# Performance work log

Measured on AMD Instinct MI355X. Metric: run time of the kernel, lower is better.

The kernel has to match this reference:

```python
import jax, jax.numpy as jnp
import numpy as np

H = 2048        # hidden_size
NH = 16         # query heads
NKV = 4         # kv heads (= NH//4, from k_proj shape H x H//4)
HD = H // NH    # head_dim = 128
B, S = 2, 2048
SCALE = 1.0 / (HD ** 0.5)


def _rope(x, cos, sin):
    # x: [B, h, S, d]; cos/sin: [S, d//2]; rotate complex pairs (even, odd)
    xr = x[..., 0::2]
    xi = x[..., 1::2]
    c = cos[None, None, :x.shape[2], :]
    s = sin[None, None, :x.shape[2], :]
    out_r = xr * c - xi * s
    out_i = xr * s + xi * c
    return jnp.stack([out_r, out_i], axis=-1).reshape(x.shape)


def setup_inputs() -> dict:
    key = jax.random.key(0)
    ks = jax.random.split(key, 6)
    hidden_states = jax.random.normal(ks[0], (B, S, H), dtype=jnp.float32)
    # RoPE table (theta = 10000), head_dim//2 frequencies
    inv_freq = 1.0 / (10000.0 ** (np.arange(0, HD, 2, dtype=np.float32) / HD))
    angles = np.arange(S, dtype=np.float32)[:, None] * inv_freq[None, :]
    freqs_cos = jnp.asarray(np.cos(angles), dtype=jnp.float32)
    freqs_sin = jnp.asarray(np.sin(angles), dtype=jnp.float32)
    w = 0.02  # keep activations in a sane range
    Wq = jax.random.normal(ks[1], (H, H), dtype=jnp.float32) * w
    Wk = jax.random.normal(ks[2], (H // 4, H), dtype=jnp.float32) * w
    Wv = jax.random.normal(ks[3], (H // 4, H), dtype=jnp.float32) * w
    Wo = jax.random.normal(ks[4], (H, H), dtype=jnp.float32) * w
    return {"hidden_states": hidden_states, "freqs_cos": freqs_cos,
            "freqs_sin": freqs_sin, "Wq": Wq, "Wk": Wk, "Wv": Wv, "Wo": Wo}


def reference(hidden_states, freqs_cos, freqs_sin, Wq, Wk, Wv, Wo):
    b, s, _ = hidden_states.shape
    q = hidden_states @ Wq.T                      # [B,S,H]
    k = hidden_states @ Wk.T                      # [B,S,H/4]
    v = hidden_states @ Wv.T                      # [B,S,H/4]
    q = q.reshape(b, s, NH, HD).transpose(0, 2, 1, 3)    # [B,NH,S,HD]
    k = k.reshape(b, s, NKV, HD).transpose(0, 2, 1, 3)   # [B,NKV,S,HD]
    v = v.reshape(b, s, NKV, HD).transpose(0, 2, 1, 3)
    q = _rope(q, freqs_cos, freqs_sin)
    k = _rope(k, freqs_cos, freqs_sin)
    # GQA: each kv head serves NH//NKV query heads
    k_rep = jnp.repeat(k, NH // NKV, axis=1)      # [B,NH,S,HD]
    v_rep = jnp.repeat(v, NH // NKV, axis=1)
    scores = jnp.einsum('bhqd,bhkd->bhqk', q, k_rep) * SCALE  # [B,NH,S,S]
    probs = jax.nn.softmax(scores, axis=-1)
    out = jnp.einsum('bhqk,bhkd->bhqd', probs, v_rep)         # [B,NH,S,HD]
    out = out.transpose(0, 2, 1, 3).reshape(b, s, H)
    return out @ Wo.T
```

## Files before the change

kernel.cpp:

```cpp
#include <hip/hip_runtime.h>

typedef __bf16 bf16_t;
typedef bf16_t bf16x8 __attribute__((ext_vector_type(8)));
typedef bf16_t bf16x4 __attribute__((ext_vector_type(4)));
typedef bf16_t bf16x2 __attribute__((ext_vector_type(2)));
typedef float f32x4 __attribute__((ext_vector_type(4)));
typedef unsigned int u32x4 __attribute__((ext_vector_type(4)));

typedef const __attribute__((address_space(1))) void* as1_cvp;
typedef __attribute__((address_space(3))) void* as3_vp;

__device__ __forceinline__ void gload16(const void* g, void* l) {
  __builtin_amdgcn_global_load_lds((as1_cvp)g, (as3_vp)l, 16, 0, 0);
}

__global__ __launch_bounds__(256) void cvt_kernel(const float* __restrict__ src,
                                                  bf16_t* __restrict__ dst, int n8) {
  int i = blockIdx.x * 256 + threadIdx.x;
  if (i >= n8) return;
  int idx = i * 8;
  float4 a = *(const float4*)(src + idx);
  float4 b = *(const float4*)(src + idx + 4);
  bf16x8 o;
  o[0] = (bf16_t)a.x; o[1] = (bf16_t)a.y; o[2] = (bf16_t)a.z; o[3] = (bf16_t)a.w;
  o[4] = (bf16_t)b.x; o[5] = (bf16_t)b.y; o[6] = (bf16_t)b.z; o[7] = (bf16_t)b.w;
  *(bf16x8*)(dst + idx) = o;
}

#define BM 128
#define BN 128
#define BK 64

__global__ __launch_bounds__(256, 2) void gemm_bt(const bf16_t* __restrict__ A,
                                                  const bf16_t* __restrict__ B,
                                                  float* __restrict__ C,
                                                  int M, int N, int K) {
  __shared__ alignas(16) bf16_t As[BM * BK];
  __shared__ alignas(16) bf16_t Bs[BN * BK];
  const int t = threadIdx.x;
  const int lane = t & 63, w = t >> 6;
  const int wm = w >> 1, wn = w & 1;
  const int lr = lane & 15, lg = lane >> 4;
  const int m0 = blockIdx.y * BM, n0 = blockIdx.x * BN;
  const int srow = t >> 3, scol = (t & 7) * 8;

  f32x4 acc[4][4] = {};

  for (int kb = 0; kb < K; kb += BK) {
    __syncthreads();
#pragma unroll
    for (int i = 0; i < 4; ++i) {
      gload16(A + (size_t)(m0 + srow + 32 * i) * K + kb + scol, As + i * 2048 + t * 8);
      gload16(B + (size_t)(n0 + srow + 32 * i) * K + kb + scol, Bs + i * 2048 + t * 8);
    }
    __syncthreads();
#pragma unroll
    for (int kk = 0; kk < 2; ++kk) {
      const int ko = kk * 32 + lg * 8;
      bf16x8 af[4], bfr[4];
#pragma unroll
      for (int r = 0; r < 4; ++r)
        af[r] = *(const bf16x8*)(As + (wm * 64 + r * 16 + lr) * BK + ko);
#pragma unroll
      for (int c = 0; c < 4; ++c)
        bfr[c] = *(const bf16x8*)(Bs + (wn * 64 + c * 16 + lr) * BK + ko);
#pragma unroll
      for (int r = 0; r < 4; ++r)
#pragma unroll
        for (int c = 0; c < 4; ++c)
          acc[r][c] = __builtin_amdgcn_mfma_f32_16x16x32_bf16(af[r], bfr[c], acc[r][c], 0, 0, 0);
    }
  }
#pragma unroll
  for (int r = 0; r < 4; ++r)
#pragma unroll
    for (int c = 0; c < 4; ++c)
#pragma unroll
      for (int b = 0; b < 4; ++b)
        C[(size_t)(m0 + wm * 64 + r * 16 + lg * 4 + b) * N + n0 + wn * 64 + c * 16 + lr] =
            acc[r][c][b];
}

__global__ __launch_bounds__(256, 2) void gemm_qkv(const bf16_t* __restrict__ A,
                                                   const bf16_t* __restrict__ B,
                                                   const float* __restrict__ cs,
                                                   const float* __restrict__ sn,
                                                   bf16_t* __restrict__ qr,
                                                   bf16_t* __restrict__ kr,
                                                   bf16_t* __restrict__ vt) {
  __shared__ alignas(16) bf16_t As[BM * BK];
  __shared__ alignas(16) bf16_t Bs[BN * BK];
  const int K = 2048;
  const int t = threadIdx.x;
  const int lane = t & 63, w = t >> 6;
  const int wm = w >> 1, wn = w & 1;
  const int lr = lane & 15, lg = lane >> 4;
  const int m0 = blockIdx.y * BM, n0 = blockIdx.x * BN;
  const int srow = t >> 3, scol = (t & 7) * 8;

  f32x4 acc[4][4] = {};

  for (int kb = 0; kb < K; kb += BK) {
    __syncthreads();
#pragma unroll
    for (int i = 0; i < 4; ++i) {
      gload16(A + (size_t)(m0 + srow + 32 * i) * K + kb + scol, As + i * 2048 + t * 8);
      gload16(B + (size_t)(n0 + srow + 32 * i) * K + kb + scol, Bs + i * 2048 + t * 8);
    }
    __syncthreads();
#pragma unroll
    for (int kk = 0; kk < 2; ++kk) {
      const int ko = kk * 32 + lg * 8;
      bf16x8 af[4], bfr[4];
#pragma unroll
      for (int r = 0; r < 4; ++r)
        af[r] = *(const bf16x8*)(As + (wm * 64 + r * 16 + lr) * BK + ko);
#pragma unroll
      for (int c = 0; c < 4; ++c)
        bfr[c] = *(const bf16x8*)(Bs + (wn * 64 + c * 16 + lr) * BK + ko);
#pragma unroll
      for (int r = 0; r < 4; ++r)
#pragma unroll
        for (int c = 0; c < 4; ++c)
          acc[r][c] = __builtin_amdgcn_mfma_f32_16x16x32_bf16(af[r], bfr[c], acc[r][c], 0, 0, 0);
    }
  }

  const int head = n0 >> 7;
  const int bb2 = m0 >> 11;
  const int sbase = (m0 & 2047) + wm * 64 + lg * 4;
  if (head < 20) {
    bf16_t* dst = (head < 16) ? qr + (size_t)(bb2 * 16 + head) * 2048 * 128
                              : kr + (size_t)(bb2 * 4 + (head - 16)) * 2048 * 128;
    const bool evn = (lr & 1) == 0;
#pragma unroll
    for (int r = 0; r < 4; ++r)
#pragma unroll
      for (int c = 0; c < 4; ++c) {
        const int cw = wn * 64 + c * 16 + lr;
        const int dix = cw >> 1;
#pragma unroll
        for (int b = 0; b < 4; ++b) {
          const int s = sbase + r * 16 + b;
          float own = acc[r][c][b];
          float prt = __shfl_xor(own, 1);
          if (evn) {
            float cc = cs[s * 64 + dix];
            float ssn = sn[s * 64 + dix];
            bf16x2 pr;
            pr[0] = (bf16_t)(own * cc - prt * ssn);
            pr[1] = (bf16_t)(own * ssn + prt * cc);
            *(bf16x2*)(dst + (size_t)s * 128 + cw) = pr;
          }
        }
      }
  } else {
    bf16_t* dst = vt + (size_t)(bb2 * 4 + (head - 20)) * 128 * 2048;
#pragma unroll
    for (int r = 0; r < 4; ++r)
#pragma unroll
      for (int c = 0; c < 4; ++c) {
        const int cw = wn * 64 + c * 16 + lr;
        const int s = sbase + r * 16;
        bf16x4 v4;
#pragma unroll
        for (int b = 0; b < 4; ++b) v4[b] = (bf16_t)acc[r][c][b];
        *(bf16x4*)(dst + (size_t)cw * 2048 + s) = v4;
      }
  }
}

#define KVB 64
__global__ __launch_bounds__(256, 4) void attn_kernel(const bf16_t* __restrict__ Q,
                                                      const bf16_t* __restrict__ Kg,
                                                      const bf16_t* __restrict__ Vg,
                                                      bf16_t* __restrict__ O) {
  __shared__ alignas(16) bf16_t Ks[KVB * 128];
  __shared__ alignas(16) bf16_t Vs[128 * KVB];
  const int t = threadIdx.x;
  const int lane = t & 63, w = t >> 6;
  const int lr = lane & 15, lg = lane >> 4;
  const int swz = (lr & 7) * 8;
  const int bid = ((blockIdx.x & 7) << 7) | (blockIdx.x >> 3);
  const int qt = bid & 31;
  const int h = (bid >> 5) & 15;
  const int bb = bid >> 9;
  const int kvh = h >> 2;

  const bf16_t* Qh = Q + (((size_t)bb * 16 + h) * 2048 + qt * 64 + w * 16) * 128;
  const bf16_t* Kh = Kg + ((size_t)bb * 4 + kvh) * 2048 * 128;
  const bf16_t* Vh = Vg + ((size_t)bb * 4 + kvh) * 128 * 2048;

  const int krow = t >> 4;
  const int kcs = ((t & 15) ^ (krow & 7)) * 8;
  const int vrow = t >> 3;
  const int vcs = ((t & 7) ^ (vrow & 7)) * 8;

  bf16x8 qf[4];
#pragma unroll
  for (int kc = 0; kc < 4; ++kc)
    qf[kc] = *(const bf16x8*)(Qh + lr * 128 + kc * 32 + lg * 8);

  f32x4 o[8] = {};
  float m2 = -1e30f;
  float ls = 0.f;
  const float sm = 0.08838834764831845f * 1.44269504088896f;

  bf16x8 kreg[4];

#define KREG_LOAD(kb)                                                                   \
  _Pragma("unroll") for (int i = 0; i < 4; ++i)                                         \
    kreg[i] = *(const bf16x8*)(Kh + (size_t)((kb) + i * 16 + krow) * 128 + kcs);
#define KDS_WRITE()                                                                     \
  _Pragma("unroll") for (int i = 0; i < 4; ++i)                                         \
    *(bf16x8*)(Ks + i * 2048 + t * 8) = kreg[i];
#define STAGE_V(kb)                                                                     \
  _Pragma("unroll") for (int i = 0; i < 4; ++i)                                         \
    gload16(Vh + (size_t)(i * 32 + vrow) * 2048 + (kb) + vcs, Vs + i * 2048 + t * 8);

  STAGE_V(0);
  KREG_LOAD(0);
  KDS_WRITE();
  KREG_LOAD(KVB);
  __syncthreads();

  for (int tt = 0; tt < 32; ++tt) {
    f32x4 sc[4];
    __builtin_amdgcn_s_setprio(1);
#pragma unroll
    for (int cg = 0; cg < 4; ++cg) {
      f32x4 a = {};
#pragma unroll
      for (int kc = 0; kc < 4; ++kc) {
        bf16x8 kf = *(const bf16x8*)(Ks + (cg * 16 + lr) * 128 + ((kc * 32 + lg * 8) ^ swz));
        a = __builtin_amdgcn_mfma_f32_16x16x32_bf16(kf, qf[kc], a, 0, 0, 0);
      }
      sc[cg] = a * sm;
    }
    __builtin_amdgcn_s_setprio(0);

    float mx = fmaxf(fmaxf(fmaxf(sc[0][0], sc[0][1]), fmaxf(sc[0][2], sc[0][3])),
                     fmaxf(fmaxf(sc[1][0], sc[1][1]), fmaxf(sc[1][2], sc[1][3])));
    mx = fmaxf(mx, fmaxf(fmaxf(fmaxf(sc[2][0], sc[2][1]), fmaxf(sc[2][2], sc[2][3])),
                         fmaxf(fmaxf(sc[3][0], sc[3][1]), fmaxf(sc[3][2], sc[3][3]))));
    mx = fmaxf(mx, __shfl_xor(mx, 16));
    mx = fmaxf(mx, __shfl_xor(mx, 32));

    if (__any(mx > m2 + 8.0f)) {
      float mn = fmaxf(m2, mx);
      float resc = exp2f(m2 - mn);
      m2 = mn;
      ls *= resc;
      float rb[4];
#pragma unroll
      for (int b = 0; b < 4; ++b) rb[b] = __shfl(resc, lg * 4 + b);
#pragma unroll
      for (int d = 0; d < 8; ++d)
#pragma unroll
        for (int b = 0; b < 4; ++b) o[d][b] *= rb[b];
    }
#pragma unroll
    for (int cg = 0; cg < 4; ++cg)
#pragma unroll
      for (int b = 0; b < 4; ++b) {
        float p = exp2f(sc[cg][b] - m2);
        sc[cg][b] = p;
        ls += p;
      }

    unsigned W[8];
#pragma unroll
    for (int cg = 0; cg < 4; ++cg)
#pragma unroll
      for (int hh2 = 0; hh2 < 2; ++hh2) {
        bf16x2 pr = {(bf16_t)sc[cg][2 * hh2], (bf16_t)sc[cg][2 * hh2 + 1]};
        W[cg * 2 + hh2] = __builtin_bit_cast(unsigned, pr);
      }
    u32x4 pw[2];
#pragma unroll
    for (int kk = 0; kk < 2; ++kk)
#pragma unroll
      for (int m = 0; m < 4; ++m) {
        int srcl = lr + 16 * (2 * (lg & 1) + (m >> 1));
        int t0 = __shfl((int)W[(2 * kk) * 2 + (m & 1)], srcl);
        int t1 = __shfl((int)W[(2 * kk + 1) * 2 + (m & 1)], srcl);
        pw[kk][m] = (unsigned)((lg & 2) ? t1 : t0);
      }
    bf16x8 pf0 = __builtin_bit_cast(bf16x8, pw[0]);
    bf16x8 pf1 = __builtin_bit_cast(bf16x8, pw[1]);

    __syncthreads();

    if (tt < 31) { KDS_WRITE(); }

    __builtin_amdgcn_s_setprio(1);
#pragma unroll
    for (int d = 0; d < 8; ++d) {
      bf16x8 vf0 = *(const bf16x8*)(Vs + (d * 16 + lr) * KVB + ((lg * 8) ^ swz));
      o[d] = __builtin_amdgcn_mfma_f32_16x16x32_bf16(pf0, vf0, o[d], 0, 0, 0);
      bf16x8 vf1 = *(const bf16x8*)(Vs + (d * 16 + lr) * KVB + ((32 + lg * 8) ^ swz));
      o[d] = __builtin_amdgcn_mfma_f32_16x16x32_bf16(pf1, vf1, o[d], 0, 0, 0);
    }
    __builtin_amdgcn_s_setprio(0);
    __syncthreads();

    if (tt < 31) { STAGE_V((tt + 1) * KVB); }
    if (tt < 30) { KREG_LOAD((tt + 2) * KVB); }
  }

  float lt = ls;
  lt += __shfl_xor(lt, 16);
  lt += __shfl_xor(lt, 32);
  float rinv[4];
#pragma unroll
  for (int b = 0; b < 4; ++b) rinv[b] = 1.0f / __shfl(lt, lg * 4 + b);
  const size_t q0 = (size_t)bb * 2048 + qt * 64 + w * 16;
#pragma unroll
  for (int d = 0; d < 8; ++d)
#pragma unroll
    for (int b = 0; b < 4; ++b) {
      float val = o[d][b] * rinv[b];
      O[(q0 + lg * 4 + b) * 2048 + h * 128 + d * 16 + lr] = (bf16_t)val;
    }
}

extern "C" void kernel_launch(void* const* d_in, const int* in_sizes, int n_in,
                              void* d_out, int out_size, void* d_ws, size_t ws_size,
                              hipStream_t stream) {
  const float* hs = (const float*)d_in[0];
  const float* fc = (const float*)d_in[1];
  const float* fs = (const float*)d_in[2];
  const float* Wq = (const float*)d_in[3];
  const float* Wk = (const float*)d_in[4];
  const float* Wv = (const float*)d_in[5];
  const float* Wo = (const float*)d_in[6];
  float* out = (float*)d_out;

  char* ws = (char*)d_ws;
  bf16_t* hs_b = (bf16_t*)ws;
  bf16_t* wcat = (bf16_t*)(ws + 16777216);
  bf16_t* wo_b = (bf16_t*)(ws + 29360128);
  bf16_t* qr = (bf16_t*)(ws + 37748736);
  bf16_t* kr = (bf16_t*)(ws + 54525952);
  bf16_t* vt = (bf16_t*)(ws + 58720256);
  bf16_t* ao = (bf16_t*)(ws + 62914560);

  cvt_kernel<<<8388608 / 8 / 256, 256, 0, stream>>>(hs, hs_b, 8388608 / 8);
  cvt_kernel<<<4194304 / 8 / 256, 256, 0, stream>>>(Wq, wcat, 4194304 / 8);
  cvt_kernel<<<1048576 / 8 / 256, 256, 0, stream>>>(Wk, wcat + 4194304, 1048576 / 8);
  cvt_kernel<<<1048576 / 8 / 256, 256, 0, stream>>>(Wv, wcat + 5242880, 1048576 / 8);
  cvt_kernel<<<4194304 / 8 / 256, 256, 0, stream>>>(Wo, wo_b, 4194304 / 8);

  dim3 g1(3072 / BN, 4096 / BM);
  gemm_qkv<<<g1, 256, 0, stream>>>(hs_b, wcat, fc, fs, qr, kr, vt);

  attn_kernel<<<1024, 256, 0, stream>>>(qr, kr, vt, ao);

  dim3 g2(2048 / BN, 4096 / BM);
  gemm_bt<<<g2, 256, 0, stream>>>(ao, wo_b, out, 4096, 2048, 2048);
}
```

Measured before the change: 261.2 us.

## Process two query row-groups per wave and double-buffer K via direct LDS loads

```diff
diff --git a/kernel.cpp b/kernel.cpp
--- a/kernel.cpp
+++ b/kernel.cpp
@@ -171,23 +171,23 @@
 }
 
 #define KVB 64
-__global__ __launch_bounds__(256, 4) void attn_kernel(const bf16_t* __restrict__ Q,
+__global__ __launch_bounds__(256, 2) void attn_kernel(const bf16_t* __restrict__ Q,
                                                       const bf16_t* __restrict__ Kg,
                                                       const bf16_t* __restrict__ Vg,
                                                       bf16_t* __restrict__ O) {
-  __shared__ alignas(16) bf16_t Ks[KVB * 128];
+  __shared__ alignas(16) bf16_t Ks[2][KVB * 128];
   __shared__ alignas(16) bf16_t Vs[128 * KVB];
   const int t = threadIdx.x;
   const int lane = t & 63, w = t >> 6;
   const int lr = lane & 15, lg = lane >> 4;
   const int swz = (lr & 7) * 8;
-  const int bid = ((blockIdx.x & 7) << 7) | (blockIdx.x >> 3);
-  const int qt = bid & 31;
-  const int h = (bid >> 5) & 15;
-  const int bb = bid >> 9;
+  const int bid = ((blockIdx.x & 7) << 6) | (blockIdx.x >> 3);
+  const int qt = bid & 15;
+  const int h = (bid >> 4) & 15;
+  const int bb = bid >> 8;
   const int kvh = h >> 2;
 
-  const bf16_t* Qh = Q + (((size_t)bb * 16 + h) * 2048 + qt * 64 + w * 16) * 128;
+  const bf16_t* Qh = Q + (((size_t)bb * 16 + h) * 2048 + qt * 128 + w * 32) * 128;
   const bf16_t* Kh = Kg + ((size_t)bb * 4 + kvh) * 2048 * 128;
   const bf16_t* Vh = Vg + ((size_t)bb * 4 + kvh) * 128 * 2048;
 
@@ -196,132 +196,143 @@
   const int vrow = t >> 3;
   const int vcs = ((t & 7) ^ (vrow & 7)) * 8;
 
-  bf16x8 qf[4];
-#pragma unroll
-  for (int kc = 0; kc < 4; ++kc)
-    qf[kc] = *(const bf16x8*)(Qh + lr * 128 + kc * 32 + lg * 8);
-
-  f32x4 o[8] = {};
-  float m2 = -1e30f;
-  float ls = 0.f;
+  bf16x8 qf[2][4];
+#pragma unroll
+  for (int rg = 0; rg < 2; ++rg)
+#pragma unroll
+    for (int kc = 0; kc < 4; ++kc)
+      qf[rg][kc] = *(const bf16x8*)(Qh + (rg * 16 + lr) * 128 + kc * 32 + lg * 8);
+
+  f32x4 o[2][8] = {};
+  float m2[2] = {-1e30f, -1e30f};
+  float ls[2] = {0.f, 0.f};
   const float sm = 0.08838834764831845f * 1.44269504088896f;
 
-  bf16x8 kreg[4];
-
-#define KREG_LOAD(kb)                                                                   \
-  _Pragma("unroll") for (int i = 0; i < 4; ++i)                                         \
-    kreg[i] = *(const bf16x8*)(Kh + (size_t)((kb) + i * 16 + krow) * 128 + kcs);
-#define KDS_WRITE()                                                                     \
-  _Pragma("unroll") for (int i = 0; i < 4; ++i)                                         \
-    *(bf16x8*)(Ks + i * 2048 + t * 8) = kreg[i];
-#define STAGE_V(kb)                                                                     \
-  _Pragma("unroll") for (int i = 0; i < 4; ++i)                                         \
+#define STAGE_K(buf, kb)                                                                  \
+  _Pragma("unroll") for (int i = 0; i < 4; ++i)                                           \
+    gload16(Kh + (size_t)((kb) + i * 16 + krow) * 128 + kcs, &Ks[buf][i * 2048 + t * 8]);
+#define STAGE_V(kb)                                                                       \
+  _Pragma("unroll") for (int i = 0; i < 4; ++i)                                           \
     gload16(Vh + (size_t)(i * 32 + vrow) * 2048 + (kb) + vcs, Vs + i * 2048 + t * 8);
 
-  STAGE_V(0);
-  KREG_LOAD(0);
-  KDS_WRITE();
-  KREG_LOAD(KVB);
+  STAGE_K(0, 0);
   __syncthreads();
 
   for (int tt = 0; tt < 32; ++tt) {
-    f32x4 sc[4];
+    const int cur = tt & 1;
+    STAGE_V(tt * KVB);
+    if (tt < 31) { STAGE_K(cur ^ 1, (tt + 1) * KVB); }
+    const bf16_t* Kc = Ks[cur];
+
+    f32x4 sc[2][4];
     __builtin_amdgcn_s_setprio(1);
 #pragma unroll
     for (int cg = 0; cg < 4; ++cg) {
-      f32x4 a = {};
+      f32x4 a0 = {}, a1 = {};
 #pragma unroll
       for (int kc = 0; kc < 4; ++kc) {
-        bf16x8 kf = *(const bf16x8*)(Ks + (cg * 16 + lr) * 128 + ((kc * 32 + lg * 8) ^ swz));
-        a = __builtin_amdgcn_mfma_f32_16x16x32_bf16(kf, qf[kc], a, 0, 0, 0);
-      }
-      sc[cg] = a * sm;
+        bf16x8 kf = *(const bf16x8*)(Kc + (cg * 16 + lr) * 128 + ((kc * 32 + lg * 8) ^ swz));
+        a0 = __builtin_amdgcn_mfma_f32_16x16x32_bf16(kf, qf[0][kc], a0, 0, 0, 0);
+        a1 = __builtin_amdgcn_mfma_f32_16x16x32_bf16(kf, qf[1][kc], a1, 0, 0, 0);
+      }
+      sc[0][cg] = a0 * sm;
+      sc[1][cg] = a1 * sm;
     }
     __builtin_amdgcn_s_setprio(0);
 
-    float mx = fmaxf(fmaxf(fmaxf(sc[0][0], sc[0][1]), fmaxf(sc[0][2], sc[0][3])),
-                     fmaxf(fmaxf(sc[1][0], sc[1][1]), fmaxf(sc[1][2], sc[1][3])));
-    mx = fmaxf(mx, fmaxf(fmaxf(fmaxf(sc[2][0], sc[2][1]), fmaxf(sc[2][2], sc[2][3])),
-                         fmaxf(fmaxf(sc[3][0], sc[3][1]), fmaxf(sc[3][2], sc[3][3]))));
-    mx = fmaxf(mx, __shfl_xor(mx, 16));
-    mx = fmaxf(mx, __shfl_xor(mx, 32));
-
-    if (__any(mx > m2 + 8.0f)) {
-      float mn = fmaxf(m2, mx);
-      float resc = exp2f(m2 - mn);
-      m2 = mn;
-      ls *= resc;
-      float rb[4];
-#pragma unroll
-      for (int b = 0; b < 4; ++b) rb[b] = __shfl(resc, lg * 4 + b);
-#pragma unroll
-      for (int d = 0; d < 8; ++d)
-#pragma unroll
-        for (int b = 0; b < 4; ++b) o[d][b] *= rb[b];
-    }
-#pragma unroll
-    for (int cg = 0; cg < 4; ++cg)
-#pragma unroll
-      for (int b = 0; b < 4; ++b) {
-        float p = exp2f(sc[cg][b] - m2);
-        sc[cg][b] = p;
-        ls += p;
-      }
-
-    unsigned W[8];
-#pragma unroll
-    for (int cg = 0; cg < 4; ++cg)
-#pragma unroll
-      for (int hh2 = 0; hh2 < 2; ++hh2) {
-        bf16x2 pr = {(bf16_t)sc[cg][2 * hh2], (bf16_t)sc[cg][2 * hh2 + 1]};
-        W[cg * 2 + hh2] = __builtin_bit_cast(unsigned, pr);
-      }
-    u32x4 pw[2];
-#pragma unroll
-    for (int kk = 0; kk < 2; ++kk)
-#pragma unroll
-      for (int m = 0; m < 4; ++m) {
-        int srcl = lr + 16 * (2 * (lg & 1) + (m >> 1));
-        int t0 = __shfl((int)W[(2 * kk) * 2 + (m & 1)], srcl);
-        int t1 = __shfl((int)W[(2 * kk + 1) * 2 + (m & 1)], srcl);
-        pw[kk][m] = (unsigned)((lg & 2) ? t1 : t0);
-      }
-    bf16x8 pf0 = __builtin_bit_cast(bf16x8, pw[0]);
-    bf16x8 pf1 = __builtin_bit_cast(bf16x8, pw[1]);
-
-    __syncthreads();
-
-    if (tt < 31) { KDS_WRITE(); }
+    float mx[2];
+#pragma unroll
+    for (int rg = 0; rg < 2; ++rg) {
+      float v = fmaxf(fmaxf(fmaxf(sc[rg][0][0], sc[rg][0][1]), fmaxf(sc[rg][0][2], sc[rg][0][3])),
+                      fmaxf(fmaxf(sc[rg][1][0], sc[rg][1][1]), fmaxf(sc[rg][1][2], sc[rg][1][3])));
+      v = fmaxf(v, fmaxf(fmaxf(fmaxf(sc[rg][2][0], sc[rg][2][1]), fmaxf(sc[rg][2][2], sc[rg][2][3])),
+                         fmaxf(fmaxf(sc[rg][3][0], sc[rg][3][1]), fmaxf(sc[rg][3][2], sc[rg][3][3]))));
+      v = fmaxf(v, __shfl_xor(v, 16));
+      v = fmaxf(v, __shfl_xor(v, 32));
+      mx[rg] = v;
+    }
+    if (__any((mx[0] > m2[0] + 8.0f) || (mx[1] > m2[1] + 8.0f))) {
+#pragma unroll
+      for (int rg = 0; rg < 2; ++rg) {
+        float mn = fmaxf(m2[rg], mx[rg]);
+        float resc = exp2f(m2[rg] - mn);
+        m2[rg] = mn;
+        ls[rg] *= resc;
+        float rb[4];
+#pragma unroll
+        for (int b = 0; b < 4; ++b) rb[b] = __shfl(resc, lg * 4 + b);
+#pragma unroll
+        for (int d = 0; d < 8; ++d)
+#pragma unroll
+          for (int b = 0; b < 4; ++b) o[rg][d][b] *= rb[b];
+      }
+    }
+    bf16x8 pf[2][2];
+#pragma unroll
+    for (int rg = 0; rg < 2; ++rg) {
+#pragma unroll
+      for (int cg = 0; cg < 4; ++cg)
+#pragma unroll
+        for (int b = 0; b < 4; ++b) {
+          float p = exp2f(sc[rg][cg][b] - m2[rg]);
+          sc[rg][cg][b] = p;
+          ls[rg] += p;
+        }
+      unsigned W[8];
+#pragma unroll
+      for (int cg = 0; cg < 4; ++cg)
+#pragma unroll
+        for (int hh2 = 0; hh2 < 2; ++hh2) {
+          bf16x2 pr = {(bf16_t)sc[rg][cg][2 * hh2], (bf16_t)sc[rg][cg][2 * hh2 + 1]};
+          W[cg * 2 + hh2] = __builtin_bit_cast(unsigned, pr);
+        }
+      u32x4 pw[2];
+#pragma unroll
+      for (int kk = 0; kk < 2; ++kk)
+#pragma unroll
+        for (int m = 0; m < 4; ++m) {
+          int srcl = lr + 16 * (2 * (lg & 1) + (m >> 1));
+          int t0 = __shfl((int)W[(2 * kk) * 2 + (m & 1)], srcl);
+          int t1 = __shfl((int)W[(2 * kk + 1) * 2 + (m & 1)], srcl);
+          pw[kk][m] = (unsigned)((lg & 2) ? t1 : t0);
+        }
+      pf[rg][0] = __builtin_bit_cast(bf16x8, pw[0]);
+      pf[rg][1] = __builtin_bit_cast(bf16x8, pw[1]);
+    }
+
+    __syncthreads();
 
     __builtin_amdgcn_s_setprio(1);
 #pragma unroll
     for (int d = 0; d < 8; ++d) {
       bf16x8 vf0 = *(const bf16x8*)(Vs + (d * 16 + lr) * KVB + ((lg * 8) ^ swz));
-      o[d] = __builtin_amdgcn_mfma_f32_16x16x32_bf16(pf0, vf0, o[d], 0, 0, 0);
+      o[0][d] = __builtin_amdgcn_mfma_f32_16x16x32_bf16(pf[0][0], vf0, o[0][d], 0, 0, 0);
+      o[1][d] = __builtin_amdgcn_mfma_f32_16x16x32_bf16(pf[1][0], vf0, o[1][d], 0, 0, 0);
       bf16x8 vf1 = *(const bf16x8*)(Vs + (d * 16 + lr) * KVB + ((32 + lg * 8) ^ swz));
-      o[d] = __builtin_amdgcn_mfma_f32_16x16x32_bf16(pf1, vf1, o[d], 0, 0, 0);
+      o[0][d] = __builtin_amdgcn_mfma_f32_16x16x32_bf16(pf[0][1], vf1, o[0][d], 0, 0, 0);
+      o[1][d] = __builtin_amdgcn_mfma_f32_16x16x32_bf16(pf[1][1], vf1, o[1][d], 0, 0, 0);
     }
     __builtin_amdgcn_s_setprio(0);
     __syncthreads();
-
-    if (tt < 31) { STAGE_V((tt + 1) * KVB); }
-    if (tt < 30) { KREG_LOAD((tt + 2) * KVB); }
-  }
-
-  float lt = ls;
-  lt += __shfl_xor(lt, 16);
-  lt += __shfl_xor(lt, 32);
-  float rinv[4];
-#pragma unroll
-  for (int b = 0; b < 4; ++b) rinv[b] = 1.0f / __shfl(lt, lg * 4 + b);
-  const size_t q0 = (size_t)bb * 2048 + qt * 64 + w * 16;
-#pragma unroll
-  for (int d = 0; d < 8; ++d)
-#pragma unroll
-    for (int b = 0; b < 4; ++b) {
-      float val = o[d][b] * rinv[b];
-      O[(q0 + lg * 4 + b) * 2048 + h * 128 + d * 16 + lr] = (bf16_t)val;
-    }
+  }
+
+  const size_t q0 = (size_t)bb * 2048 + qt * 128 + w * 32;
+#pragma unroll
+  for (int rg = 0; rg < 2; ++rg) {
+    float lt = ls[rg];
+    lt += __shfl_xor(lt, 16);
+    lt += __shfl_xor(lt, 32);
+    float rinv[4];
+#pragma unroll
+    for (int b = 0; b < 4; ++b) rinv[b] = 1.0f / __shfl(lt, lg * 4 + b);
+#pragma unroll
+    for (int d = 0; d < 8; ++d)
+#pragma unroll
+      for (int b = 0; b < 4; ++b) {
+        float val = o[rg][d][b] * rinv[b];
+        O[(q0 + rg * 16 + lg * 4 + b) * 2048 + h * 128 + d * 16 + lr] = (bf16_t)val;
+      }
+  }
 }
 
 extern "C" void kernel_launch(void* const* d_in, const int* in_sizes, int n_in,
@@ -354,7 +365,7 @@
   dim3 g1(3072 / BN, 4096 / BM);
   gemm_qkv<<<g1, 256, 0, stream>>>(hs_b, wcat, fc, fs, qr, kr, vt);
 
-  attn_kernel<<<1024, 256, 0, stream>>>(qr, kr, vt, ao);
+  attn_kernel<<<512, 256, 0, stream>>>(qr, kr, vt, ao);
 
   dim3 g2(2048 / BN, 4096 / BM);
   gemm_bt<<<g2, 256, 0, stream>>>(ao, wo_b, out, 4096, 2048, 2048);
```

Result: faster. 244.6 us (-6.4%).

## Switch attention to 32x32x16 MFMA with 128-row query tiles and double-buffered K

Applied to the files above, without the earlier changes.

```diff
diff --git a/kernel.cpp b/kernel.cpp
--- a/kernel.cpp
+++ b/kernel.cpp
@@ -5,6 +5,7 @@
 typedef bf16_t bf16x4 __attribute__((ext_vector_type(4)));
 typedef bf16_t bf16x2 __attribute__((ext_vector_type(2)));
 typedef float f32x4 __attribute__((ext_vector_type(4)));
+typedef float f32x16 __attribute__((ext_vector_type(16)));
 typedef unsigned int u32x4 __attribute__((ext_vector_type(4)));
 
 typedef const __attribute__((address_space(1))) void* as1_cvp;
@@ -12,6 +13,10 @@
 
 __device__ __forceinline__ void gload16(const void* g, void* l) {
   __builtin_amdgcn_global_load_lds((as1_cvp)g, (as3_vp)l, 16, 0, 0);
+}
+
+__device__ __forceinline__ unsigned pxor32(unsigned x) {
+  return (unsigned)__shfl_xor((int)x, 32);
 }
 
 __global__ __launch_bounds__(256) void cvt_kernel(const float* __restrict__ src,
@@ -171,79 +176,72 @@
 }
 
 #define KVB 64
-__global__ __launch_bounds__(256, 4) void attn_kernel(const bf16_t* __restrict__ Q,
+__global__ __launch_bounds__(256, 2) void attn_kernel(const bf16_t* __restrict__ Q,
                                                       const bf16_t* __restrict__ Kg,
                                                       const bf16_t* __restrict__ Vg,
                                                       bf16_t* __restrict__ O) {
-  __shared__ alignas(16) bf16_t Ks[KVB * 128];
-  __shared__ alignas(16) bf16_t Vs[128 * KVB];
+  __shared__ alignas(16) bf16_t Ks[2][16 * KVB * 8];
+  __shared__ alignas(16) bf16_t Vs[8 * 128 * 8];
   const int t = threadIdx.x;
   const int lane = t & 63, w = t >> 6;
-  const int lr = lane & 15, lg = lane >> 4;
-  const int swz = (lr & 7) * 8;
-  const int bid = ((blockIdx.x & 7) << 7) | (blockIdx.x >> 3);
-  const int qt = bid & 31;
-  const int h = (bid >> 5) & 15;
-  const int bb = bid >> 9;
+  const int l31 = lane & 31, hi = lane >> 5;
+  const int bid = ((blockIdx.x & 7) << 6) | (blockIdx.x >> 3);
+  const int qt = bid & 15;
+  const int h = (bid >> 4) & 15;
+  const int bb = bid >> 8;
   const int kvh = h >> 2;
 
-  const bf16_t* Qh = Q + (((size_t)bb * 16 + h) * 2048 + qt * 64 + w * 16) * 128;
+  const bf16_t* Qh = Q + (((size_t)bb * 16 + h) * 2048 + qt * 128 + w * 32) * 128;
   const bf16_t* Kh = Kg + ((size_t)bb * 4 + kvh) * 2048 * 128;
   const bf16_t* Vh = Vg + ((size_t)bb * 4 + kvh) * 128 * 2048;
 
-  const int krow = t >> 4;
-  const int kcs = ((t & 15) ^ (krow & 7)) * 8;
-  const int vrow = t >> 3;
-  const int vcs = ((t & 7) ^ (vrow & 7)) * 8;
-
-  bf16x8 qf[4];
-#pragma unroll
-  for (int kc = 0; kc < 4; ++kc)
-    qf[kc] = *(const bf16x8*)(Qh + lr * 128 + kc * 32 + lg * 8);
-
-  f32x4 o[8] = {};
+  bf16x8 qf[8];
+#pragma unroll
+  for (int c = 0; c < 8; ++c)
+    qf[c] = *(const bf16x8*)(Qh + l31 * 128 + c * 16 + hi * 8);
+
+  f32x16 o[4] = {};
   float m2 = -1e30f;
   float ls = 0.f;
   const float sm = 0.08838834764831845f * 1.44269504088896f;
 
-  bf16x8 kreg[4];
-
-#define KREG_LOAD(kb)                                                                   \
+#define STAGE_K(buf, kb)                                                                \
   _Pragma("unroll") for (int i = 0; i < 4; ++i)                                         \
-    kreg[i] = *(const bf16x8*)(Kh + (size_t)((kb) + i * 16 + krow) * 128 + kcs);
-#define KDS_WRITE()                                                                     \
-  _Pragma("unroll") for (int i = 0; i < 4; ++i)                                         \
-    *(bf16x8*)(Ks + i * 2048 + t * 8) = kreg[i];
+    gload16(Kh + (size_t)((kb) + (t & 63)) * 128 + (i * 4 + (t >> 6)) * 8,              \
+            &Ks[buf][(i * 256 + t) * 8]);
 #define STAGE_V(kb)                                                                     \
   _Pragma("unroll") for (int i = 0; i < 4; ++i)                                         \
-    gload16(Vh + (size_t)(i * 32 + vrow) * 2048 + (kb) + vcs, Vs + i * 2048 + t * 8);
-
-  STAGE_V(0);
-  KREG_LOAD(0);
-  KDS_WRITE();
-  KREG_LOAD(KVB);
+    gload16(Vh + (size_t)(t & 127) * 2048 + (kb) + (i * 2 + (t >> 7)) * 8,              \
+            &Vs[(i * 256 + t) * 8]);
+
+  STAGE_K(0, 0);
   __syncthreads();
 
   for (int tt = 0; tt < 32; ++tt) {
-    f32x4 sc[4];
+    const int cur = tt & 1;
+    STAGE_V(tt * KVB);
+    if (tt < 31) { STAGE_K(cur ^ 1, (tt + 1) * KVB); }
+    const bf16_t* Kc = Ks[cur];
+
+    f32x16 s0 = {}, s1 = {};
     __builtin_amdgcn_s_setprio(1);
 #pragma unroll
-    for (int cg = 0; cg < 4; ++cg) {
-      f32x4 a = {};
-#pragma unroll
-      for (int kc = 0; kc < 4; ++kc) {
-        bf16x8 kf = *(const bf16x8*)(Ks + (cg * 16 + lr) * 128 + ((kc * 32 + lg * 8) ^ swz));
-        a = __builtin_amdgcn_mfma_f32_16x16x32_bf16(kf, qf[kc], a, 0, 0, 0);
-      }
-      sc[cg] = a * sm;
+    for (int c = 0; c < 8; ++c) {
+      bf16x8 kf0 = *(const bf16x8*)(Kc + ((c * 2 + hi) * 64 + l31) * 8);
+      bf16x8 kf1 = *(const bf16x8*)(Kc + ((c * 2 + hi) * 64 + 32 + l31) * 8);
+      s0 = __builtin_amdgcn_mfma_f32_32x32x16_bf16(kf0, qf[c], s0, 0, 0, 0);
+      s1 = __builtin_amdgcn_mfma_f32_32x32x16_bf16(kf1, qf[c], s1, 0, 0, 0);
     }
     __builtin_amdgcn_s_setprio(0);
-
-    float mx = fmaxf(fmaxf(fmaxf(sc[0][0], sc[0][1]), fmaxf(sc[0][2], sc[0][3])),
-                     fmaxf(fmaxf(sc[1][0], sc[1][1]), fmaxf(sc[1][2], sc[1][3])));
-    mx = fmaxf(mx, fmaxf(fmaxf(fmaxf(sc[2][0], sc[2][1]), fmaxf(sc[2][2], sc[2][3])),
-                         fmaxf(fmaxf(sc[3][0], sc[3][1]), fmaxf(sc[3][2], sc[3][3]))));
-    mx = fmaxf(mx, __shfl_xor(mx, 16));
+    s0 = s0 * sm;
+    s1 = s1 * sm;
+
+    float tm[8];
+#pragma unroll
+    for (int j = 0; j < 8; ++j)
+      tm[j] = fmaxf(fmaxf(s0[2 * j], s0[2 * j + 1]), fmaxf(s1[2 * j], s1[2 * j + 1]));
+    float mx = fmaxf(fmaxf(fmaxf(tm[0], tm[1]), fmaxf(tm[2], tm[3])),
+                     fmaxf(fmaxf(tm[4], tm[5]), fmaxf(tm[6], tm[7])));
     mx = fmaxf(mx, __shfl_xor(mx, 32));
 
     if (__any(mx > m2 + 8.0f)) {
@@ -251,76 +249,83 @@
       float resc = exp2f(m2 - mn);
       m2 = mn;
       ls *= resc;
-      float rb[4];
-#pragma unroll
-      for (int b = 0; b < 4; ++b) rb[b] = __shfl(resc, lg * 4 + b);
-#pragma unroll
-      for (int d = 0; d < 8; ++d)
-#pragma unroll
-        for (int b = 0; b < 4; ++b) o[d][b] *= rb[b];
-    }
-#pragma unroll
-    for (int cg = 0; cg < 4; ++cg)
-#pragma unroll
-      for (int b = 0; b < 4; ++b) {
-        float p = exp2f(sc[cg][b] - m2);
-        sc[cg][b] = p;
-        ls += p;
+      float rf[16];
+#pragma unroll
+      for (int r = 0; r < 16; ++r) rf[r] = __shfl(resc, (r & 3) + 8 * (r >> 2) + 4 * hi);
+#pragma unroll
+      for (int dblk = 0; dblk < 4; ++dblk)
+#pragma unroll
+        for (int r = 0; r < 16; ++r) o[dblk][r] *= rf[r];
+    }
+#pragma unroll
+    for (int r = 0; r < 16; ++r) {
+      float p0 = exp2f(s0[r] - m2);
+      float p1 = exp2f(s1[r] - m2);
+      s0[r] = p0; s1[r] = p1;
+      ls += p0 + p1;
+    }
+
+    unsigned Wa[8], Wb[8];
+#pragma unroll
+    for (int s = 0; s < 8; ++s) {
+      bf16x2 a = {(bf16_t)s0[2 * s], (bf16_t)s0[2 * s + 1]};
+      bf16x2 b = {(bf16_t)s1[2 * s], (bf16_t)s1[2 * s + 1]};
+      Wa[s] = __builtin_bit_cast(unsigned, a);
+      Wb[s] = __builtin_bit_cast(unsigned, b);
+    }
+    bf16x8 pf[4];
+    {
+      unsigned wv[16];
+#pragma unroll
+      for (int g = 0; g < 4; ++g) {
+        unsigned* W = (g & 2) ? Wb : Wa;
+        const int o4 = (g & 1) * 4;
+        unsigned pp0 = pxor32(W[o4 + 0]);
+        unsigned pp1 = pxor32(W[o4 + 1]);
+        unsigned pp2 = pxor32(W[o4 + 2]);
+        unsigned pp3 = pxor32(W[o4 + 3]);
+        wv[g * 4 + 0] = hi ? pp2 : W[o4 + 0];
+        wv[g * 4 + 1] = hi ? pp3 : W[o4 + 1];
+        wv[g * 4 + 2] = hi ? W[o4 + 2] : pp0;
+        wv[g * 4 + 3] = hi ? W[o4 + 3] : pp1;
       }
-
-    unsigned W[8];
-#pragma unroll
-    for (int cg = 0; cg < 4; ++cg)
-#pragma unroll
-      for (int hh2 = 0; hh2 < 2; ++hh2) {
-        bf16x2 pr = {(bf16_t)sc[cg][2 * hh2], (bf16_t)sc[cg][2 * hh2 + 1]};
-        W[cg * 2 + hh2] = __builtin_bit_cast(unsigned, pr);
+      u32x4 pw0 = {wv[0], wv[1], wv[2], wv[3]};
+      u32x4 pw1 = {wv[4], wv[5], wv[6], wv[7]};
+      u32x4 pw2 = {wv[8], wv[9], wv[10], wv[11]};
+      u32x4 pw3 = {wv[12], wv[13], wv[14], wv[15]};
+      pf[0] = __builtin_bit_cast(bf16x8, pw0);
+      pf[1] = __builtin_bit_cast(bf16x8, pw1);
+      pf[2] = __builtin_bit_cast(bf16x8, pw2);
+      pf[3] = __builtin_bit_cast(bf16x8, pw3);
+    }
+
+    __syncthreads();
+
+    __builtin_amdgcn_s_setprio(1);
+#pragma unroll
+    for (int kk = 0; kk < 4; ++kk) {
+#pragma unroll
+      for (int dblk = 0; dblk < 4; ++dblk) {
+        bf16x8 vf = *(const bf16x8*)(Vs + ((kk * 2 + hi) * 128 + dblk * 32 + l31) * 8);
+        o[dblk] = __builtin_amdgcn_mfma_f32_32x32x16_bf16(pf[kk], vf, o[dblk], 0, 0, 0);
       }
-    u32x4 pw[2];
-#pragma unroll
-    for (int kk = 0; kk < 2; ++kk)
-#pragma unroll
-      for (int m = 0; m < 4; ++m) {
-        int srcl = lr + 16 * (2 * (lg & 1) + (m >> 1));
-        int t0 = __shfl((int)W[(2 * kk) * 2 + (m & 1)], srcl);
-        int t1 = __shfl((int)W[(2 * kk + 1) * 2 + (m & 1)], srcl);
-        pw[kk][m] = (unsigned)((lg & 2) ? t1 : t0);
-      }
-    bf16x8 pf0 = __builtin_bit_cast(bf16x8, pw[0]);
-    bf16x8 pf1 = __builtin_bit_cast(bf16x8, pw[1]);
-
-    __syncthreads();
-
-    if (tt < 31) { KDS_WRITE(); }
-
-    __builtin_amdgcn_s_setprio(1);
-#pragma unroll
-    for (int d = 0; d < 8; ++d) {
-      bf16x8 vf0 = *(const bf16x8*)(Vs + (d * 16 + lr) * KVB + ((lg * 8) ^ swz));
-      o[d] = __builtin_amdgcn_mfma_f32_16x16x32_bf16(pf0, vf0, o[d], 0, 0, 0);
-      bf16x8 vf1 = *(const bf16x8*)(Vs + (d * 16 + lr) * KVB + ((32 + lg * 8) ^ swz));
-      o[d] = __builtin_amdgcn_mfma_f32_16x16x32_bf16(pf1, vf1, o[d], 0, 0, 0);
     }
     __builtin_amdgcn_s_setprio(0);
     __syncthreads();
-
-    if (tt < 31) { STAGE_V((tt + 1) * KVB); }
-    if (tt < 30) { KREG_LOAD((tt + 2) * KVB); }
   }
 
-  float lt = ls;
-  lt += __shfl_xor(lt, 16);
-  lt += __shfl_xor(lt, 32);
-  float rinv[4];
-#pragma unroll
-  for (int b = 0; b < 4; ++b) rinv[b] = 1.0f / __shfl(lt, lg * 4 + b);
-  const size_t q0 = (size_t)bb * 2048 + qt * 64 + w * 16;
-#pragma unroll
-  for (int d = 0; d < 8; ++d)
-#pragma unroll
-    for (int b = 0; b < 4; ++b) {
-      float val = o[d][b] * rinv[b];
-      O[(q0 + lg * 4 + b) * 2048 + h * 128 + d * 16 + lr] = (bf16_t)val;
+  float lt = ls + __shfl_xor(ls, 32);
+  float rinv = 1.0f / lt;
+  float rq[16];
+#pragma unroll
+  for (int r = 0; r < 16; ++r) rq[r] = __shfl(rinv, (r & 3) + 8 * (r >> 2) + 4 * hi);
+  const size_t q0 = (size_t)bb * 2048 + qt * 128 + w * 32;
+#pragma unroll
+  for (int dblk = 0; dblk < 4; ++dblk)
+#pragma unroll
+    for (int r = 0; r < 16; ++r) {
+      const int qrow = (r & 3) + 8 * (r >> 2) + 4 * hi;
+      O[(q0 + qrow) * 2048 + h * 128 + dblk * 32 + l31] = (bf16_t)(o[dblk][r] * rq[r]);
     }
 }
 
@@ -354,7 +359,7 @@
   dim3 g1(3072 / BN, 4096 / BM);
   gemm_qkv<<<g1, 256, 0, stream>>>(hs_b, wcat, fc, fs, qr, kr, vt);
 
-  attn_kernel<<<1024, 256, 0, stream>>>(qr, kr, vt, ao);
+  attn_kernel<<<512, 256, 0, stream>>>(qr, kr, vt, ao);
 
   dim3 g2(2048 / BN, 4096 / BM);
   gemm_bt<<<g2, 256, 0, stream>>>(ao, wo_b, out, 4096, 2048, 2048);
```

After: 246.4 us. -5.7%, faster.
